# Optimization experiments

Measured on AMD Instinct MI355X. Metric: run time of the kernel, lower is better.

Reference implementation:

```python
import jax, jax.numpy as jnp
import numpy as np
from jax import lax

D_MODEL = 128

def _pad_same(x, kh, kw):
    ph, pw = kh - 1, kw - 1
    return jnp.pad(x, ((0, 0), (0, 0), (ph // 2, ph - ph // 2), (pw // 2, pw - pw // 2)))

def _conv(x, w, b):
    y = lax.conv_general_dilated(x, w, (1, 1), 'VALID', dimension_numbers=('NCHW', 'OIHW', 'NCHW'))
    return y + b[None, :, None, None]

def _group_norm(x, g, b, groups, eps=1e-5):
    N, C, H, W = x.shape
    xr = x.reshape(N, groups, -1)
    m = xr.mean(axis=2, keepdims=True)
    v = xr.var(axis=2, keepdims=True)
    xn = ((xr - m) / jnp.sqrt(v + eps)).reshape(N, C, H, W)
    return xn * g[None, :, None, None] + b[None, :, None, None]

def _maxpool(x, kh, kw):
    return lax.reduce_window(x, -jnp.inf, lax.max, (1, 1, kh, kw), (1, 1, kh, kw), 'VALID')

def _l2norm(x, axis):
    # torch F.normalize(p=2): x / max(||x||, eps)
    return x / jnp.maximum(jnp.linalg.norm(x, axis=axis, keepdims=True), 1e-12)

def _pos_encoding(S, d):
    pos = jnp.arange(S, dtype=jnp.float32)[:, None]
    div = jnp.exp(jnp.arange(0, d, 2, dtype=jnp.float32) * (-float(np.log(10000.0)) / d))
    pe = jnp.zeros((S, d), dtype=jnp.float32)
    pe = pe.at[:, 0::2].set(jnp.sin(pos * div)).at[:, 1::2].set(jnp.cos(pos * div))
    return pe

def setup_inputs() -> dict:
    key = jax.random.key(0)
    ks = jax.random.split(key, 16)
    def w(k, shape, fan_in):
        return jax.random.normal(k, shape, dtype=jnp.float32) * (1.0 / np.sqrt(fan_in))
    return {
        'x': jax.random.normal(ks[0], (1, 1024, 72, 64), dtype=jnp.float32),
        'conv1_w': w(ks[1], (32, 1, 6, 4), 1 * 6 * 4),
        'conv1_b': jnp.zeros((32,), jnp.float32),
        'gn1_g': jnp.ones((32,), jnp.float32), 'gn1_b': jnp.zeros((32,), jnp.float32),
        'conv2_w': w(ks[2], (64, 32, 6, 4), 32 * 6 * 4),
        'conv2_b': jnp.zeros((64,), jnp.float32),
        'gn2_g': jnp.ones((64,), jnp.float32), 'gn2_b': jnp.zeros((64,), jnp.float32),
        'conv3_w': w(ks[3], (128, 64, 6, 4), 64 * 6 * 4),
        'conv3_b': jnp.zeros((128,), jnp.float32),
        'gn3_g': jnp.ones((128,), jnp.float32), 'gn3_b': jnp.zeros((128,), jnp.float32),
        'fc1_w': w(ks[4], (128, 1024), 1024),
        'fc1_b': jnp.zeros((128,), jnp.float32),
        'wq': w(ks[5], (128, 128), 128), 'bq': jnp.zeros((128,), jnp.float32),
        'wk': w(ks[6], (128, 128), 128), 'bk': jnp.zeros((128,), jnp.float32),
        'wv': w(ks[7], (128, 128), 128), 'bv': jnp.zeros((128,), jnp.float32),
    }

def reference(x, conv1_w, conv1_b, gn1_g, gn1_b, conv2_w, conv2_b, gn2_g, gn2_b,
              conv3_w, conv3_b, gn3_g, gn3_b, fc1_w, fc1_b, wq, bq, wk, bk, wv, bv):
    selu = jax.nn.selu
    # x: [1, S, 72, 64] -> transpose(0,1): [S, 1, 72, 64] (S frames, 1 channel)
    h = jnp.transpose(x, (1, 0, 2, 3))
    h = _maxpool(_group_norm(selu(_conv(_pad_same(h, 6, 4), conv1_w, conv1_b)), gn1_g, gn1_b, 32), 2, 4)
    h = _maxpool(_group_norm(selu(_conv(_pad_same(h, 6, 4), conv2_w, conv2_b)), gn2_g, gn2_b, 32), 3, 4)
    h = _maxpool(_group_norm(selu(_conv(_pad_same(h, 6, 4), conv3_w, conv3_b)), gn3_g, gn3_b, 32), 3, 2)
    e = h.reshape(h.shape[0], -1)                       # [S, 1024]
    e = _l2norm(selu(e @ fc1_w.T + fc1_b), axis=1)      # [S, 128]
    S = e.shape[0]
    q = selu(e @ wq.T + bq)
    k = selu(e @ wk.T + bk)
    v = selu(e @ wv.T + bv)
    k_pos = k + _pos_encoding(S, D_MODEL)               # PE added to K only
    attn = jax.nn.softmax((q @ k_pos.T) / jnp.sqrt(jnp.float32(D_MODEL)), axis=-1)  # [S, S]
    # torch F.normalize default dim=1 on [1,S,D] -> normalize over the sequence axis
    out = _l2norm(attn @ v, axis=0) + e
    ea = _l2norm(out, axis=0)                           # [S, 128]
    # pairwise L2 distances (self-similarity matrix), then 1 - d/max(d)
    sq = jnp.sum(ea * ea, axis=1)
    d2 = jnp.maximum(sq[:, None] + sq[None, :] - 2.0 * (ea @ ea.T), 0.0)
    d = jnp.sqrt(d2 + 1e-12)
    return 1.0 - d / jnp.max(d)
```

## Files before the change

kernel.cpp:

```cpp
#include <hip/hip_runtime.h>
#include <hip/hip_bf16.h>
#include <math.h>

#define SELU_SCALE 1.0507009873554805f
#define SELU_SA    1.7580993408473766f

typedef __attribute__((ext_vector_type(8))) short short8;
typedef __attribute__((ext_vector_type(4))) short short4v;
typedef __attribute__((ext_vector_type(4))) float f32x4;

__device__ __forceinline__ float selu_f(float x){
    return x > 0.f ? SELU_SCALE * x : fmaf(SELU_SA, __expf(x), -SELU_SA);
}

__device__ __forceinline__ unsigned short bfc(float v){
    __hip_bfloat16 h = __float2bfloat16(v);
    return __builtin_bit_cast(unsigned short, h);
}
__device__ __forceinline__ float f_bf(unsigned short u){
    unsigned int x = ((unsigned int)u) << 16;
    return __builtin_bit_cast(float, x);
}

__device__ __forceinline__ float warp_sum(float v){
    #pragma unroll
    for(int o=32;o>0;o>>=1) v += __shfl_down(v,o,64);
    return v;
}
__device__ __forceinline__ float warp_max(float v){
    #pragma unroll
    for(int o=32;o>0;o>>=1) v = fmaxf(v,__shfl_down(v,o,64));
    return v;
}

__device__ __forceinline__ void block_sum2(float &a, float &b, float* sred, int nw){
    int lane = threadIdx.x & 63, w = threadIdx.x >> 6;
    a = warp_sum(a); b = warp_sum(b);
    __syncthreads();
    if(lane==0){ sred[w]=a; sred[16+w]=b; }
    __syncthreads();
    if(w==0){
        float x = (lane<nw)? sred[lane] : 0.f;
        float y = (lane<nw)? sred[16+lane] : 0.f;
        x = warp_sum(x); y = warp_sum(y);
        if(lane==0){ sred[0]=x; sred[16]=y; }
    }
    __syncthreads();
    a = sred[0]; b = sred[16];
}

__device__ __forceinline__ float block_max_f(float v, float* sred, int nw){
    int lane = threadIdx.x & 63, w = threadIdx.x >> 6;
    v = warp_max(v);
    __syncthreads();
    if(lane==0) sred[w]=v;
    __syncthreads();
    if(w==0){
        float x = (lane<nw)? sred[lane] : -INFINITY;
        x = warp_max(x);
        if(lane==0) sred[0]=x;
    }
    __syncthreads();
    return sred[0];
}

__global__ void k_prep(const float* __restrict__ f1w, const float* __restrict__ wq,
                       const float* __restrict__ wk, const float* __restrict__ wv,
                       const float* __restrict__ w1, const float* __restrict__ w2,
                       const float* __restrict__ w3,
                       float* __restrict__ wt, float* __restrict__ wqt,
                       float* __restrict__ wkt, float* __restrict__ wvt,
                       short* __restrict__ w1bf, short* __restrict__ w2bf,
                       short* __restrict__ w3bf){
    int idx = blockIdx.x*256 + threadIdx.x;
    if(idx < 131072){ int r = idx >> 10, cc = idx & 1023; wt[cc*128 + r] = f1w[idx]; return; }
    idx -= 131072;
    if(idx < 16384){ int r = idx >> 7, cc = idx & 127; wqt[cc*128 + r] = wq[idx]; return; }
    idx -= 16384;
    if(idx < 16384){ int r = idx >> 7, cc = idx & 127; wkt[cc*128 + r] = wk[idx]; return; }
    idx -= 16384;
    if(idx < 16384){ int r = idx >> 7, cc = idx & 127; wvt[cc*128 + r] = wv[idx]; return; }
    idx -= 16384;
    if(idx < 49152){
        int t = idx >> 11, rem = idx & 2047;
        int oc = rem >> 5, ic = rem & 31;
        w2bf[idx] = (short)bfc(w2[oc*768 + ic*24 + t]);
        return;
    }
    idx -= 49152;
    if(idx < 196608){
        int t = idx >> 13, rem = idx & 8191;
        int oc = rem >> 6, ic = rem & 63;
        w3bf[idx] = (short)bfc(w3[oc*1536 + ic*24 + t]);
        return;
    }
    idx -= 196608;
    if(idx < 1024){
        int oc = idx >> 5, k = idx & 31;
        w1bf[idx] = (k < 24) ? (short)bfc(w1[oc*24 + k]) : (short)0;
    }
}

__global__ __launch_bounds__(768,1) void k_conv1m(
    const float* __restrict__ x, const short* __restrict__ w1bf,
    const float* __restrict__ bias, const float* __restrict__ g,
    const float* __restrict__ be, float* __restrict__ out)
{
    int s = blockIdx.x, tid = threadIdx.x;
    int l = tid & 63, wv = tid >> 6;
    int c = l & 15, qr = l >> 4;
    __shared__ char smem[127728];
    short* sdup = (short*)smem;
    char* pmaxb = smem + 41712;
    char* pminb = smem + 83184;
    float* sredf = (float*)(smem + 124656);
    __shared__ float scsh[64];

    const float* xs = x + (size_t)s*4608;
    for(int i = tid; i < 5056; i += 768){
        int yp = i >> 6, xx = i & 63;
        unsigned long long pk = 0ull;
        if(yp >= 2 && yp < 74){
            const float* row = xs + (yp-2)*64;
            #pragma unroll
            for(int t=0;t<4;t++){
                int cp = xx + t;
                float f = (cp>=1 && cp<65) ? row[cp-1] : 0.f;
                pk |= (unsigned long long)bfc(f) << (16*t);
            }
        }
        *(unsigned long long*)((char*)sdup + yp*528 + (xx&3)*128 + (xx>>2)*8) = pk;
    }
    short8 a0 = *(const short8*)(w1bf + c*32 + qr*8);
    short8 a1 = *(const short8*)(w1bf + (16+c)*32 + qr*8);
    float bias8[8];
    #pragma unroll
    for(int t=0;t<2;t++)
        #pragma unroll
        for(int r=0;r<4;r++) bias8[t*4+r] = bias[t*16 + qr*4 + r];
    float ssum8[8], ssq8[8];
    #pragma unroll
    for(int i=0;i<8;i++){ ssum8[i]=0.f; ssq8[i]=0.f; }
    __syncthreads();

    #pragma unroll 1
    for(int u=0; u<3; u++){
        int py = wv*3 + u;
        float pmx[8], pmn[8];
        #pragma unroll
        for(int i=0;i<8;i++){ pmx[i]=-INFINITY; pmn[i]=INFINITY; }
        #pragma unroll
        for(int off=0; off<4; off++){
            const char* bb = (const char*)sdup + off*128 + c*8;
            #pragma unroll
            for(int rr=0; rr<2; rr++){
                int y = py*2 + rr;
                short4v lo = *(const short4v*)(bb + (y+2*qr)*528);
                short4v hi = *(const short4v*)(bb + (y+2*qr+1)*528);
                short8 bfrag = __builtin_shufflevector(lo, hi, 0,1,2,3,4,5,6,7);
                f32x4 d0 = __builtin_amdgcn_mfma_f32_16x16x32_bf16(a0, bfrag, (f32x4){0.f,0.f,0.f,0.f}, 0,0,0);
                f32x4 d1 = __builtin_amdgcn_mfma_f32_16x16x32_bf16(a1, bfrag, (f32x4){0.f,0.f,0.f,0.f}, 0,0,0);
                #pragma unroll
                for(int r=0;r<4;r++){
                    float v0 = selu_f(d0[r] + bias8[r]);
                    float v1 = selu_f(d1[r] + bias8[4+r]);
                    ssum8[r]   += v0; ssq8[r]   = fmaf(v0,v0,ssq8[r]);
                    ssum8[4+r] += v1; ssq8[4+r] = fmaf(v1,v1,ssq8[4+r]);
                    pmx[r]   = fmaxf(pmx[r],   v0); pmn[r]   = fminf(pmn[r],   v0);
                    pmx[4+r] = fmaxf(pmx[4+r], v1); pmn[4+r] = fminf(pmn[4+r], v1);
                }
            }
        }
        int base = (py*16 + c)*72;
        #pragma unroll
        for(int t=0;t<2;t++){
            unsigned long long mpk=0ull, npk=0ull;
            #pragma unroll
            for(int r=0;r<4;r++){
                mpk |= (unsigned long long)bfc(pmx[t*4+r]) << (16*r);
                npk |= (unsigned long long)bfc(pmn[t*4+r]) << (16*r);
            }
            *(unsigned long long*)(pmaxb + base + t*32 + qr*8) = mpk;
            *(unsigned long long*)(pminb + base + t*32 + qr*8) = npk;
        }
    }
    #pragma unroll
    for(int off=1; off<16; off<<=1){
        #pragma unroll
        for(int i=0;i<8;i++){
            ssum8[i] += __shfl_xor(ssum8[i], off);
            ssq8[i]  += __shfl_xor(ssq8[i],  off);
        }
    }
    if(c == 0){
        #pragma unroll
        for(int i=0;i<8;i++){
            sredf[((wv*4 + qr)*8 + i)*2]     = ssum8[i];
            sredf[((wv*4 + qr)*8 + i)*2 + 1] = ssq8[i];
        }
    }
    __syncthreads();
    if(tid < 32){
        int oc = tid;
        int t = oc >> 4, rem = oc & 15, q = rem >> 2, r = rem & 3;
        int i = t*4 + r;
        float sum=0.f, sq=0.f;
        for(int w=0; w<12; w++){
            sum += sredf[((w*4+q)*8+i)*2];
            sq  += sredf[((w*4+q)*8+i)*2+1];
        }
        float mean = sum*(1.f/4608.f);
        float var  = sq*(1.f/4608.f) - mean*mean;
        float inv  = rsqrtf(var + 1e-5f);
        float sc = g[oc]*inv;
        scsh[oc*2]   = sc;
        scsh[oc*2+1] = be[oc] - mean*sc;
    }
    __syncthreads();
    float* ob = out + (size_t)s*18432;
    for(int i = tid; i < 18432; i += 768){
        int oc = i / 576, wpx = i - oc*576;
        float sc = scsh[oc*2], sh = scsh[oc*2+1];
        int boff = wpx*72 + oc*2;
        float vm = f_bf(*(unsigned short*)(pmaxb + boff));
        float vn = f_bf(*(unsigned short*)(pminb + boff));
        ob[i] = fmaf(sc, (sc >= 0.f) ? vm : vn, sh);
    }
}

__global__ __launch_bounds__(512,2) void k_conv2m(
    const float* __restrict__ in, const short* __restrict__ w2bf,
    const float* __restrict__ bias, const float* __restrict__ g,
    const float* __restrict__ be, float* __restrict__ out)
{
    int s = blockIdx.x, tid = threadIdx.x;
    int l = tid & 63, wv = tid >> 6;
    int ocp = wv >> 2, yq = wv & 3;
    int xc = l & 15, qr = l >> 4;
    __shared__ short sinb[26240];
    __shared__ float sred[2][4][2][4][2][2];
    int* zp = (int*)sinb;
    for(int i=tid;i<13120;i+=512) zp[i]=0;
    __syncthreads();
    const float* ibase = in + (size_t)s*18432;
    #pragma unroll
    for(int h=0;h<2;h++){
        int ic = (wv*2+h)*2;
        #pragma unroll
        for(int k=0;k<9;k++){
            int px = l + 64*k;
            float v0 = ibase[ic*576 + px];
            float v1 = ibase[(ic+1)*576 + px];
            int R = (px>>4)+2, C = (px&15)+1;
            int key = (C>>1)&3;
            int q0 = ic>>3;
            int byteoff = (R*20+C)*64 + (((q0^key)&3)<<4) + (ic&7)*2;
            *(unsigned int*)((char*)sinb + byteoff) =
                (unsigned int)bfc(v0) | ((unsigned int)bfc(v1)<<16);
        }
    }
    __syncthreads();
    f32x4 acc[2][9];
    #pragma unroll
    for(int o=0;o<2;o++)
        #pragma unroll
        for(int yt=0;yt<9;yt++) acc[o][yt] = (f32x4){0.f,0.f,0.f,0.f};
    const short8* wb = (const short8*)w2bf;
    int arow = ocp*32 + xc;
    short8 a0 = wb[arow*4 + qr];
    short8 a1 = wb[(arow+16)*4 + qr];
    char* sb = (char*)sinb;
    for(int tap=0; tap<24; tap++){
        short8 na0, na1;
        if(tap<23){
            na0 = wb[((tap+1)*64 + arow)*4 + qr];
            na1 = wb[((tap+1)*64 + arow + 16)*4 + qr];
        }
        int kh = tap>>2, kw = tap&3;
        int C = xc + kw;
        int cb = C*64 + (((qr ^ ((C>>1)&3))&3)<<4);
        int rb = (yq*9 + kh)*1280;
        #pragma unroll
        for(int yt=0;yt<9;yt++){
            short8 bf_ = *(const short8*)(sb + rb + yt*1280 + cb);
            acc[0][yt] = __builtin_amdgcn_mfma_f32_16x16x32_bf16(a0, bf_, acc[0][yt], 0,0,0);
            acc[1][yt] = __builtin_amdgcn_mfma_f32_16x16x32_bf16(a1, bf_, acc[1][yt], 0,0,0);
        }
        a0 = na0; a1 = na1;
    }
    #pragma unroll
    for(int o=0;o<2;o++){
        int ocb = (ocp*2+o)*16 + qr*4;
        float b0 = bias[ocb], b1 = bias[ocb+1], b2 = bias[ocb+2], b3 = bias[ocb+3];
        float s0=0,q0=0,s1=0,q1=0;
        #pragma unroll
        for(int yt=0;yt<9;yt++){
            float v0=selu_f(acc[o][yt][0]+b0), v1=selu_f(acc[o][yt][1]+b1);
            float v2=selu_f(acc[o][yt][2]+b2), v3=selu_f(acc[o][yt][3]+b3);
            acc[o][yt][0]=v0; acc[o][yt][1]=v1; acc[o][yt][2]=v2; acc[o][yt][3]=v3;
            s0+=v0+v1; q0+=v0*v0+v1*v1; s1+=v2+v3; q1+=v2*v2+v3*v3;
        }
        #pragma unroll
        for(int off=1;off<16;off<<=1){
            s0+=__shfl_xor(s0,off); q0+=__shfl_xor(q0,off);
            s1+=__shfl_xor(s1,off); q1+=__shfl_xor(q1,off);
        }
        if(xc==0){
            sred[ocp][yq][o][qr][0][0]=s0; sred[ocp][yq][o][qr][0][1]=q0;
            sred[ocp][yq][o][qr][1][0]=s1; sred[ocp][yq][o][qr][1][1]=q1;
        }
    }
    __syncthreads();
    float* ob = out + (size_t)s*64*48;
    #pragma unroll
    for(int o=0;o<2;o++){
        #pragma unroll
        for(int grp=0;grp<2;grp++){
            float ts=0, tq=0;
            #pragma unroll
            for(int y2=0;y2<4;y2++){ ts += sred[ocp][y2][o][qr][grp][0]; tq += sred[ocp][y2][o][qr][grp][1]; }
            float mean = ts*(1.f/1152.f);
            float var  = tq*(1.f/1152.f) - mean*mean;
            float inv  = rsqrtf(var + 1e-5f);
            int oc0 = (ocp*2+o)*16 + qr*4 + grp*2;
            float sc0 = g[oc0]*inv,   sh0 = be[oc0]   - mean*sc0;
            float sc1 = g[oc0+1]*inv, sh1 = be[oc0+1] - mean*sc1;
            #pragma unroll
            for(int yt=0;yt<9;yt++){
                acc[o][yt][grp*2]   = acc[o][yt][grp*2]*sc0 + sh0;
                acc[o][yt][grp*2+1] = acc[o][yt][grp*2+1]*sc1 + sh1;
            }
        }
        #pragma unroll
        for(int r=0;r<4;r++){
            #pragma unroll
            for(int py=0;py<3;py++){
                float m = fmaxf(fmaxf(acc[o][3*py][r],acc[o][3*py+1][r]),acc[o][3*py+2][r]);
                m = fmaxf(m, __shfl_xor(m,1));
                m = fmaxf(m, __shfl_xor(m,2));
                if((xc&3)==0){
                    int oc = (ocp*2+o)*16 + qr*4 + r;
                    ob[(size_t)oc*48 + (yq*3+py)*4 + (xc>>2)] = m;
                }
            }
        }
    }
}

__global__ __launch_bounds__(512,2) void k_conv3m(
    const float* __restrict__ in, const short* __restrict__ w3bf,
    const float* __restrict__ bias, const float* __restrict__ g,
    const float* __restrict__ be, float* __restrict__ e0)
{
    int sq = blockIdx.x, tid = threadIdx.x;
    int l = tid & 63, wv = tid >> 6;
    int ocp = wv >> 1, sL = wv & 1;
    int c = l & 15, qr = l >> 4;
    int yl = c >> 2, xl = c & 3;
    __shared__ char smem[49152];
    short* sinb = (short*)smem;
    int* zp = (int*)smem;
    for(int i=tid;i<8704;i+=512) zp[i]=0;
    __syncthreads();
    const float* ibase = in + (size_t)sq*6144;
    for(int j=0;j<6;j++){
        int idx = tid + 512*j;
        int px = idx % 48;
        int rest = idx / 48;
        int icp = rest & 31, ss = rest >> 5;
        int ic = icp*2;
        float v0 = ibase[ss*3072 + ic*48 + px];
        float v1 = ibase[ss*3072 + (ic+1)*48 + px];
        int R = (px>>2)+2, C = (px&3)+1;
        int pos = ss*136 + R*8 + C;
        int key = ((R&1)<<2) | (C&3);
        int q0 = ic>>3;
        int byteoff = pos*128 + (((q0^key)&7)<<4) + (ic&7)*2;
        *(unsigned int*)(smem + byteoff) = (unsigned int)bfc(v0) | ((unsigned int)bfc(v1)<<16);
    }
    __syncthreads();
    f32x4 acc[2][3];
    #pragma unroll
    for(int o=0;o<2;o++)
        #pragma unroll
        for(int yt=0;yt<3;yt++) acc[o][yt] = (f32x4){0.f,0.f,0.f,0.f};
    const short8* wb = (const short8*)w3bf;
    int arow = ocp*32 + c;
    char* sb = smem + sL*17408;
    short8 a0 = wb[arow*8 + qr];
    short8 a1 = wb[(arow+16)*8 + qr];
    for(int t2=0; t2<48; t2++){
        short8 na0, na1;
        if(t2<47){
            int nt = t2+1;
            na0 = wb[((nt>>1)*128 + arow)*8 + (nt&1)*4 + qr];
            na1 = wb[((nt>>1)*128 + arow + 16)*8 + (nt&1)*4 + qr];
        }
        int tap = t2>>1, ks = t2&1;
        int kh = tap>>2, kw = tap&3;
        int C = xl + kw;
        int q0 = ks*4 + qr;
        #pragma unroll
        for(int yt=0;yt<3;yt++){
            int R = yt*4 + yl + kh;
            int key = ((R&1)<<2) | (C&3);
            short8 bf_ = *(const short8*)(sb + (R*8+C)*128 + (((q0^key)&7)<<4));
            acc[0][yt] = __builtin_amdgcn_mfma_f32_16x16x32_bf16(a0, bf_, acc[0][yt], 0,0,0);
            acc[1][yt] = __builtin_amdgcn_mfma_f32_16x16x32_bf16(a1, bf_, acc[1][yt], 0,0,0);
        }
        a0 = na0; a1 = na1;
    }
    #pragma unroll
    for(int o=0;o<2;o++){
        int ocb = (ocp*2+o)*16 + qr*4;
        float b0 = bias[ocb], b1 = bias[ocb+1], b2 = bias[ocb+2], b3 = bias[ocb+3];
        float ssum=0.f, ssq=0.f;
        #pragma unroll
        for(int yt=0;yt<3;yt++){
            float v0=selu_f(acc[o][yt][0]+b0), v1=selu_f(acc[o][yt][1]+b1);
            float v2=selu_f(acc[o][yt][2]+b2), v3=selu_f(acc[o][yt][3]+b3);
            acc[o][yt][0]=v0; acc[o][yt][1]=v1; acc[o][yt][2]=v2; acc[o][yt][3]=v3;
            ssum += v0+v1+v2+v3; ssq += v0*v0+v1*v1+v2*v2+v3*v3;
        }
        #pragma unroll
        for(int off=1;off<16;off<<=1){ ssum+=__shfl_xor(ssum,off); ssq+=__shfl_xor(ssq,off); }
        float mean = ssum*(1.f/192.f);
        float var  = ssq*(1.f/192.f) - mean*mean;
        float inv  = rsqrtf(var + 1e-5f);
        #pragma unroll
        for(int r=0;r<4;r++){
            int oc = ocb + r;
            float sc = g[oc]*inv, sh = be[oc] - mean*sc;
            #pragma unroll
            for(int yt=0;yt<3;yt++) acc[o][yt][r] = acc[o][yt][r]*sc + sh;
        }
    }
    __syncthreads();
    float* scr = (float*)smem + wv*1536;
    #pragma unroll
    for(int o=0;o<2;o++)
        #pragma unroll
        for(int yt=0;yt<3;yt++)
            #pragma unroll
            for(int r=0;r<4;r++){
                int px = (yt*4+yl)*4 + xl;
                scr[o*768 + (qr*4+r)*48 + px] = acc[o][yt][r];
            }
    __syncthreads();
    float* sr = (float*)smem + wv*1536 + (l>>5)*768 + ((l>>1)&15)*48;
    int x2 = l&1;
    float* eo = e0 + (size_t)(sq*2+sL)*1024 + ((size_t)(ocp*2 + (l>>5))*16 + ((l>>1)&15))*8;
    #pragma unroll
    for(int py=0;py<4;py++){
        float m = sr[(py*3)*4 + x2*2];
        m = fmaxf(m, sr[(py*3)*4 + x2*2+1]);
        m = fmaxf(m, sr[(py*3+1)*4 + x2*2]);
        m = fmaxf(m, sr[(py*3+1)*4 + x2*2+1]);
        m = fmaxf(m, sr[(py*3+2)*4 + x2*2]);
        m = fmaxf(m, sr[(py*3+2)*4 + x2*2+1]);
        eo[py*2 + x2] = m;
    }
}

__global__ __launch_bounds__(256) void k_fcqkv(
    const float* __restrict__ e0, const float* __restrict__ wt,
    const float* __restrict__ bias, float* __restrict__ e,
    const float* __restrict__ wqt, const float* __restrict__ bq,
    const float* __restrict__ wkt, const float* __restrict__ bk,
    const float* __restrict__ wvt, const float* __restrict__ bv,
    float* __restrict__ q, float* __restrict__ kp, float* __restrict__ v)
{
    int s = blockIdx.x, tid = threadIdx.x;
    int j = tid & 127, half = tid >> 7;
    __shared__ float se[1024];
    __shared__ float sp[2][128];
    __shared__ float sred[2];
    __shared__ float se2[128];
    __shared__ float sp3[3][2][128];
    for(int i=tid;i<1024;i+=256) se[i] = e0[(size_t)s*1024+i];
    __syncthreads();
    float acc = half ? 0.f : bias[j];
    const float* wp = wt + (size_t)half*512*128 + j;
    const float* sep = se + half*512;
    #pragma unroll 8
    for(int i=0;i<512;i++) acc += sep[i]*wp[(size_t)i*128];
    sp[half][j] = acc;
    __syncthreads();
    if(half==0){
        float vv = selu_f(sp[0][j]+sp[1][j]);
        float a = vv*vv;
        #pragma unroll
        for(int o=1;o<64;o<<=1) a += __shfl_xor(a,o);
        if((j&63)==0) sred[j>>6]=a;
    }
    __syncthreads();
    if(half==0){
        float den = fmaxf(sqrtf(sred[0]+sred[1]), 1e-12f);
        float vv = selu_f(sp[0][j]+sp[1][j]);
        float ev = vv/den;
        se2[j] = ev;
        e[(size_t)s*128+j] = ev;
    }
    __syncthreads();
    float aq = half?0.f:bq[j], ak = half?0.f:bk[j], av = half?0.f:bv[j];
    int i0 = half*64;
    #pragma unroll 8
    for(int i=i0;i<i0+64;i++){
        float f = se2[i];
        aq += f*wqt[i*128+j];
        ak += f*wkt[i*128+j];
        av += f*wvt[i*128+j];
    }
    sp3[0][half][j]=aq; sp3[1][half][j]=ak; sp3[2][half][j]=av;
    __syncthreads();
    if(half==0){
        float vq = selu_f(sp3[0][0][j]+sp3[0][1][j]);
        float vk = selu_f(sp3[1][0][j]+sp3[1][1][j]);
        float vv = selu_f(sp3[2][0][j]+sp3[2][1][j]);
        int i2 = j & ~1;
        float div = __expf(-(float)i2 * 0.07195578412155481f);
        float ang = (float)s * div;
        float pe = (j & 1) ? cosf(ang) : sinf(ang);
        q[(size_t)s*128+j]  = vq;
        kp[(size_t)s*128+j] = vk + pe;
        v[(size_t)s*128+j]  = vv;
    }
}

__global__ __launch_bounds__(256) void k_attnav(
    const float* __restrict__ q, const float* __restrict__ kp,
    const float* __restrict__ v, float* __restrict__ av)
{
    int s = blockIdx.x, tid = threadIdx.x;
    __shared__ float sq_[128];
    __shared__ float sredm[32];
    __shared__ float spb[1024];
    __shared__ float spart[2][128];
    if(tid < 128) sq_[tid] = q[(size_t)s*128+tid];
    __syncthreads();
    float val[4];
    const float4* qr = (const float4*)sq_;
    #pragma unroll
    for(int k2=0;k2<4;k2++){
        int t = tid + k2*256;
        const float4* kr = (const float4*)(kp + (size_t)t*128);
        float acc=0.f;
        #pragma unroll 8
        for(int i=0;i<32;i++){
            float4 a=qr[i], b=kr[i];
            acc += a.x*b.x + a.y*b.y + a.z*b.z + a.w*b.w;
        }
        val[k2] = acc * 0.08838834764831845f;
    }
    float m = fmaxf(fmaxf(val[0],val[1]), fmaxf(val[2],val[3]));
    m = block_max_f(m,sredm,4);
    float lsum=0.f, dummy=0.f;
    #pragma unroll
    for(int k2=0;k2<4;k2++){ val[k2]=__expf(val[k2]-m); lsum+=val[k2]; }
    block_sum2(lsum,dummy,sredm,4);
    float invs = 1.f/lsum;
    #pragma unroll
    for(int k2=0;k2<4;k2++) spb[tid + k2*256] = val[k2]*invs;
    __syncthreads();
    int j = tid & 127, half = tid >> 7;
    float acc=0.f;
    int t0 = half*512;
    for(int t=t0;t<t0+512;t++) acc += spb[t]*v[(size_t)t*128+j];
    spart[half][j] = acc;
    __syncthreads();
    if(half==0) av[(size_t)s*128+j] = spart[0][j] + spart[1][j];
}

__global__ __launch_bounds__(256) void k_colpipe(
    const float* __restrict__ av, const float* __restrict__ e, float* __restrict__ ea)
{
    int j = blockIdx.x, t = threadIdx.x;
    __shared__ float sred[4];
    float v[4];
    float ss = 0.f;
    #pragma unroll
    for(int k=0;k<4;k++){
        v[k] = av[(size_t)(t + 256*k)*128 + j];
        ss += v[k]*v[k];
    }
    #pragma unroll
    for(int off=1;off<64;off<<=1) ss += __shfl_xor(ss,off);
    int lane = t & 63, w = t >> 6;
    if(lane==0) sred[w]=ss;
    __syncthreads();
    float n1 = fmaxf(sqrtf(sred[0]+sred[1]+sred[2]+sred[3]), 1e-12f);
    __syncthreads();
    float ss2 = 0.f;
    #pragma unroll
    for(int k=0;k<4;k++){
        float o = v[k]/n1 + e[(size_t)(t + 256*k)*128 + j];
        v[k] = o;
        ss2 += o*o;
    }
    #pragma unroll
    for(int off=1;off<64;off<<=1) ss2 += __shfl_xor(ss2,off);
    if(lane==0) sred[w]=ss2;
    __syncthreads();
    float n2 = fmaxf(sqrtf(sred[0]+sred[1]+sred[2]+sred[3]), 1e-12f);
    #pragma unroll
    for(int k=0;k<4;k++) ea[(size_t)(t + 256*k)*128 + j] = v[k]/n2;
}

__global__ __launch_bounds__(128) void k_sq(const float* __restrict__ ea, float* __restrict__ sq){
    int s = blockIdx.x, j = threadIdx.x;
    __shared__ float sred[32];
    float v = ea[(size_t)s*128+j];
    float a=v*v, b=0.f;
    block_sum2(a,b,sred,2);
    if(j==0) sq[s]=a;
}

__global__ __launch_bounds__(256) void k_gram(
    const float* __restrict__ ea, const float* __restrict__ sq,
    float* __restrict__ d2, unsigned int* __restrict__ maxbits)
{
    int j0 = blockIdx.x*32, i0 = blockIdx.y*32, tid = threadIdx.x;
    __shared__ float sa[32*128];
    __shared__ float sb[32*128];
    __shared__ float sred[32];
    for(int idx=tid;idx<4096;idx+=256){
        sa[idx] = ea[(size_t)i0*128 + idx];
        sb[idx] = ea[(size_t)j0*128 + idx];
    }
    __syncthreads();
    float lm = 0.f;
    #pragma unroll
    for(int k2=0;k2<4;k2++){
        int p = tid + k2*256;
        int li = p>>5, lj = p&31;
        const float4* A = (const float4*)(sa + li*128);
        const float4* B = (const float4*)(sb + lj*128);
        float acc=0.f;
        #pragma unroll 8
        for(int i=0;i<32;i++){
            float4 a=A[i], b=B[i];
            acc += a.x*b.x + a.y*b.y + a.z*b.z + a.w*b.w;
        }
        float dd = fmaxf(sq[i0+li] + sq[j0+lj] - 2.f*acc, 0.f);
        d2[(size_t)(i0+li)*1024 + j0+lj] = dd;
        lm = fmaxf(lm, dd);
    }
    lm = block_max_f(lm,sred,4);
    if(tid==0) atomicMax(maxbits, __float_as_uint(lm));
}

__global__ __launch_bounds__(256) void k_final(
    const float* __restrict__ d2, const unsigned int* __restrict__ maxbits, float* __restrict__ out)
{
    int idx = blockIdx.x*256 + threadIdx.x;
    float md = sqrtf(__uint_as_float(*maxbits) + 1e-12f);
    out[idx] = 1.f - sqrtf(d2[idx] + 1e-12f)/md;
}

extern "C" void kernel_launch(void* const* d_in, const int* in_sizes, int n_in,
                              void* d_out, int out_size, void* d_ws, size_t ws_size,
                              hipStream_t stream)
{
    const float* x   = (const float*)d_in[0];
    const float* c1w = (const float*)d_in[1];  const float* c1b = (const float*)d_in[2];
    const float* g1g = (const float*)d_in[3];  const float* g1b = (const float*)d_in[4];
    const float* c2w = (const float*)d_in[5];  const float* c2b = (const float*)d_in[6];
    const float* g2g = (const float*)d_in[7];  const float* g2b = (const float*)d_in[8];
    const float* c3w = (const float*)d_in[9];  const float* c3b = (const float*)d_in[10];
    const float* g3g = (const float*)d_in[11]; const float* g3b = (const float*)d_in[12];
    const float* f1w = (const float*)d_in[13]; const float* f1b = (const float*)d_in[14];
    const float* wq  = (const float*)d_in[15]; const float* bq  = (const float*)d_in[16];
    const float* wk  = (const float*)d_in[17]; const float* bk  = (const float*)d_in[18];
    const float* wv  = (const float*)d_in[19]; const float* bv  = (const float*)d_in[20];

    float* W = (float*)d_ws;
    float* e0   = W;
    float* avb  = W + 2097152;
    float* eab  = W + 2228224;
    float* d2b  = W + 2359296;
    float* buf1 = W;
    float* buf2 = W + 18874368;
    float* wt   = W + 22020096;
    float* wqt  = W + 22151168;
    float* wkt  = W + 22167552;
    float* wvt  = W + 22183936;
    float* eb   = W + 22200320;
    float* qb   = W + 22331392;
    float* kpb  = W + 22462464;
    float* vb   = W + 22593536;
    float* sqb  = W + 22724608;
    unsigned int* maxb = (unsigned int*)(W + 22725632);
    short* w2bf = (short*)(W + 22725648);
    short* w3bf = (short*)(W + 22750224);
    short* w1bf = (short*)(W + 22848528);

    k_prep<<<1670,256,0,stream>>>(f1w, wq, wk, wv, c1w, c2w, c3w,
                                  wt, wqt, wkt, wvt, w1bf, w2bf, w3bf);

    k_conv1m<<<1024,768,0,stream>>>(x, w1bf, c1b, g1g, g1b, buf1);
    k_conv2m<<<1024,512,0,stream>>>(buf1, w2bf, c2b, g2g, g2b, buf2);
    k_conv3m<<<512,512,0,stream>>>(buf2, w3bf, c3b, g3g, g3b, e0);

    k_fcqkv<<<1024,256,0,stream>>>(e0, wt, f1b, eb, wqt,bq, wkt,bk, wvt,bv, qb,kpb,vb);
    k_attnav<<<1024,256,0,stream>>>(qb, kpb, vb, avb);

    hipMemsetAsync(maxb, 0, 4, stream);
    k_colpipe<<<128,256,0,stream>>>(avb, eb, eab);
    k_sq<<<1024,128,0,stream>>>(eab, sqb);
    k_gram<<<dim3(32,32),256,0,stream>>>(eab, sqb, d2b, maxb);
    k_final<<<4096,256,0,stream>>>(d2b, maxb, (float*)d_out);
}
```

Before: 387.9 us.

## Batch four sequence rows per block in FC/QKV and attention, fold row norms into gram

The fc1/QKV and attention kernels now handle four sequence positions per 512-thread block, so each weight, key and value load is reused across four rows instead of one. The column-normalisation kernel uses 1024 threads with one element each. The separate squared-norm kernel is removed and its sums are computed inside the gram tile kernel from shared memory. The aim is less redundant global traffic on weights and K/V plus one fewer launch, at the cost of fewer blocks (256) in the middle stages and some repeated norm work across gram tiles.

```diff
diff --git a/kernel.cpp b/kernel.cpp
--- a/kernel.cpp
+++ b/kernel.cpp
@@ -22,46 +22,10 @@
     return __builtin_bit_cast(float, x);
 }
 
-__device__ __forceinline__ float warp_sum(float v){
-    #pragma unroll
-    for(int o=32;o>0;o>>=1) v += __shfl_down(v,o,64);
-    return v;
-}
 __device__ __forceinline__ float warp_max(float v){
     #pragma unroll
     for(int o=32;o>0;o>>=1) v = fmaxf(v,__shfl_down(v,o,64));
     return v;
-}
-
-__device__ __forceinline__ void block_sum2(float &a, float &b, float* sred, int nw){
-    int lane = threadIdx.x & 63, w = threadIdx.x >> 6;
-    a = warp_sum(a); b = warp_sum(b);
-    __syncthreads();
-    if(lane==0){ sred[w]=a; sred[16+w]=b; }
-    __syncthreads();
-    if(w==0){
-        float x = (lane<nw)? sred[lane] : 0.f;
-        float y = (lane<nw)? sred[16+lane] : 0.f;
-        x = warp_sum(x); y = warp_sum(y);
-        if(lane==0){ sred[0]=x; sred[16]=y; }
-    }
-    __syncthreads();
-    a = sred[0]; b = sred[16];
-}
-
-__device__ __forceinline__ float block_max_f(float v, float* sred, int nw){
-    int lane = threadIdx.x & 63, w = threadIdx.x >> 6;
-    v = warp_max(v);
-    __syncthreads();
-    if(lane==0) sred[w]=v;
-    __syncthreads();
-    if(w==0){
-        float x = (lane<nw)? sred[lane] : -INFINITY;
-        x = warp_max(x);
-        if(lane==0) sred[0]=x;
-    }
-    __syncthreads();
-    return sred[0];
 }
 
 __global__ void k_prep(const float* __restrict__ f1w, const float* __restrict__ wq,
@@ -462,7 +426,7 @@
     }
 }
 
-__global__ __launch_bounds__(256) void k_fcqkv(
+__global__ __launch_bounds__(512) void k_fcqkv(
     const float* __restrict__ e0, const float* __restrict__ wt,
     const float* __restrict__ bias, float* __restrict__ e,
     const float* __restrict__ wqt, const float* __restrict__ bq,
@@ -470,169 +434,202 @@
     const float* __restrict__ wvt, const float* __restrict__ bv,
     float* __restrict__ q, float* __restrict__ kp, float* __restrict__ v)
 {
-    int s = blockIdx.x, tid = threadIdx.x;
-    int j = tid & 127, half = tid >> 7;
-    __shared__ float se[1024];
-    __shared__ float sp[2][128];
-    __shared__ float sred[2];
-    __shared__ float se2[128];
-    __shared__ float sp3[3][2][128];
-    for(int i=tid;i<1024;i+=256) se[i] = e0[(size_t)s*1024+i];
-    __syncthreads();
-    float acc = half ? 0.f : bias[j];
-    const float* wp = wt + (size_t)half*512*128 + j;
-    const float* sep = se + half*512;
-    #pragma unroll 8
-    for(int i=0;i<512;i++) acc += sep[i]*wp[(size_t)i*128];
-    sp[half][j] = acc;
-    __syncthreads();
-    if(half==0){
-        float vv = selu_f(sp[0][j]+sp[1][j]);
-        float a = vv*vv;
-        #pragma unroll
-        for(int o=1;o<64;o<<=1) a += __shfl_xor(a,o);
-        if((j&63)==0) sred[j>>6]=a;
-    }
-    __syncthreads();
-    if(half==0){
-        float den = fmaxf(sqrtf(sred[0]+sred[1]), 1e-12f);
-        float vv = selu_f(sp[0][j]+sp[1][j]);
-        float ev = vv/den;
-        se2[j] = ev;
-        e[(size_t)s*128+j] = ev;
-    }
-    __syncthreads();
-    float aq = half?0.f:bq[j], ak = half?0.f:bk[j], av = half?0.f:bv[j];
-    int i0 = half*64;
-    #pragma unroll 8
-    for(int i=i0;i<i0+64;i++){
-        float f = se2[i];
-        aq += f*wqt[i*128+j];
-        ak += f*wkt[i*128+j];
-        av += f*wvt[i*128+j];
-    }
-    sp3[0][half][j]=aq; sp3[1][half][j]=ak; sp3[2][half][j]=av;
-    __syncthreads();
-    if(half==0){
-        float vq = selu_f(sp3[0][0][j]+sp3[0][1][j]);
-        float vk = selu_f(sp3[1][0][j]+sp3[1][1][j]);
-        float vv = selu_f(sp3[2][0][j]+sp3[2][1][j]);
-        int i2 = j & ~1;
-        float div = __expf(-(float)i2 * 0.07195578412155481f);
-        float ang = (float)s * div;
-        float pe = (j & 1) ? cosf(ang) : sinf(ang);
-        q[(size_t)s*128+j]  = vq;
-        kp[(size_t)s*128+j] = vk + pe;
-        v[(size_t)s*128+j]  = vv;
-    }
-}
-
-__global__ __launch_bounds__(256) void k_attnav(
+    int s0 = blockIdx.x*4, tid = threadIdx.x;
+    int j = tid & 127, q4 = tid >> 7;
+    __shared__ float se[4][1024];
+    __shared__ float sp[4][4][128];
+    __shared__ float sredn[4][2];
+    __shared__ float se2[4][128];
+    __shared__ float sp3[3][4][4][128];
+    for(int i=tid;i<4096;i+=512){
+        int sl = i >> 10, ii = i & 1023;
+        se[sl][ii] = e0[(size_t)(s0+sl)*1024 + ii];
+    }
+    __syncthreads();
+    float acc[4] = {0.f,0.f,0.f,0.f};
+    const float* wp = wt + (size_t)q4*256*128 + j;
+    const int ibase = q4*256;
+    #pragma unroll 4
+    for(int i=0;i<256;i++){
+        float w = wp[(size_t)i*128];
+        #pragma unroll
+        for(int sl=0;sl<4;sl++) acc[sl] = fmaf(se[sl][ibase+i], w, acc[sl]);
+    }
+    #pragma unroll
+    for(int sl=0;sl<4;sl++) sp[sl][q4][j] = acc[sl];
+    __syncthreads();
+    int sl2 = q4, lane = tid & 63, wv_ = tid >> 6;
+    float vfc = selu_f(bias[j] + sp[sl2][0][j] + sp[sl2][1][j] + sp[sl2][2][j] + sp[sl2][3][j]);
+    float a = vfc*vfc;
+    #pragma unroll
+    for(int o=1;o<64;o<<=1) a += __shfl_xor(a, o);
+    if(lane==0) sredn[sl2][wv_&1] = a;
+    __syncthreads();
+    float den = fmaxf(sqrtf(sredn[sl2][0]+sredn[sl2][1]), 1e-12f);
+    float ev = vfc/den;
+    se2[sl2][j] = ev;
+    e[(size_t)(s0+sl2)*128 + j] = ev;
+    __syncthreads();
+    float aq[4]={0,0,0,0}, ak[4]={0,0,0,0}, av[4]={0,0,0,0};
+    int i0b = q4*32;
+    #pragma unroll 4
+    for(int i=0;i<32;i++){
+        float wqv = wqt[(i0b+i)*128 + j];
+        float wkv = wkt[(i0b+i)*128 + j];
+        float wvv = wvt[(i0b+i)*128 + j];
+        #pragma unroll
+        for(int sl=0;sl<4;sl++){
+            float f = se2[sl][i0b+i];
+            aq[sl] = fmaf(f, wqv, aq[sl]);
+            ak[sl] = fmaf(f, wkv, ak[sl]);
+            av[sl] = fmaf(f, wvv, av[sl]);
+        }
+    }
+    #pragma unroll
+    for(int sl=0;sl<4;sl++){
+        sp3[0][sl][q4][j] = aq[sl];
+        sp3[1][sl][q4][j] = ak[sl];
+        sp3[2][sl][q4][j] = av[sl];
+    }
+    __syncthreads();
+    float vq = selu_f(bq[j] + sp3[0][sl2][0][j]+sp3[0][sl2][1][j]+sp3[0][sl2][2][j]+sp3[0][sl2][3][j]);
+    float vk = selu_f(bk[j] + sp3[1][sl2][0][j]+sp3[1][sl2][1][j]+sp3[1][sl2][2][j]+sp3[1][sl2][3][j]);
+    float vv = selu_f(bv[j] + sp3[2][sl2][0][j]+sp3[2][sl2][1][j]+sp3[2][sl2][2][j]+sp3[2][sl2][3][j]);
+    int i2 = j & ~1;
+    float dv = __expf(-(float)i2 * 0.07195578412155481f);
+    float ang = (float)(s0+sl2) * dv;
+    float pe = (j & 1) ? cosf(ang) : sinf(ang);
+    q[(size_t)(s0+sl2)*128+j]  = vq;
+    kp[(size_t)(s0+sl2)*128+j] = vk + pe;
+    v[(size_t)(s0+sl2)*128+j]  = vv;
+}
+
+__global__ __launch_bounds__(512) void k_attnav(
     const float* __restrict__ q, const float* __restrict__ kp,
     const float* __restrict__ v, float* __restrict__ av)
 {
-    int s = blockIdx.x, tid = threadIdx.x;
-    __shared__ float sq_[128];
-    __shared__ float sredm[32];
-    __shared__ float spb[1024];
-    __shared__ float spart[2][128];
-    if(tid < 128) sq_[tid] = q[(size_t)s*128+tid];
-    __syncthreads();
-    float val[4];
-    const float4* qr = (const float4*)sq_;
-    #pragma unroll
-    for(int k2=0;k2<4;k2++){
-        int t = tid + k2*256;
+    int s0 = blockIdx.x*4, tid = threadIdx.x;
+    __shared__ float4 sq4[4][32];
+    __shared__ float p[4][1024];
+    __shared__ float spart[4][4][128];
+    __shared__ float smx[4][2], ssm[4][2];
+    ((float*)sq4)[tid] = q[(size_t)s0*128 + tid];
+    __syncthreads();
+    #pragma unroll
+    for(int h=0;h<2;h++){
+        int t = tid + h*512;
         const float4* kr = (const float4*)(kp + (size_t)t*128);
-        float acc=0.f;
-        #pragma unroll 8
+        float d[4] = {0.f,0.f,0.f,0.f};
+        #pragma unroll 4
         for(int i=0;i<32;i++){
-            float4 a=qr[i], b=kr[i];
-            acc += a.x*b.x + a.y*b.y + a.z*b.z + a.w*b.w;
-        }
-        val[k2] = acc * 0.08838834764831845f;
-    }
-    float m = fmaxf(fmaxf(val[0],val[1]), fmaxf(val[2],val[3]));
-    m = block_max_f(m,sredm,4);
-    float lsum=0.f, dummy=0.f;
-    #pragma unroll
-    for(int k2=0;k2<4;k2++){ val[k2]=__expf(val[k2]-m); lsum+=val[k2]; }
-    block_sum2(lsum,dummy,sredm,4);
-    float invs = 1.f/lsum;
-    #pragma unroll
-    for(int k2=0;k2<4;k2++) spb[tid + k2*256] = val[k2]*invs;
-    __syncthreads();
-    int j = tid & 127, half = tid >> 7;
-    float acc=0.f;
-    int t0 = half*512;
-    for(int t=t0;t<t0+512;t++) acc += spb[t]*v[(size_t)t*128+j];
-    spart[half][j] = acc;
-    __syncthreads();
-    if(half==0) av[(size_t)s*128+j] = spart[0][j] + spart[1][j];
-}
-
-__global__ __launch_bounds__(256) void k_colpipe(
+            float4 kv = kr[i];
+            #pragma unroll
+            for(int sl=0;sl<4;sl++){
+                float4 qv = sq4[sl][i];
+                d[sl] += kv.x*qv.x + kv.y*qv.y + kv.z*qv.z + kv.w*qv.w;
+            }
+        }
+        #pragma unroll
+        for(int sl=0;sl<4;sl++) p[sl][t] = d[sl]*0.08838834764831845f;
+    }
+    __syncthreads();
+    int sl2 = tid>>7, t2 = tid&127, lane = tid&63, wv_ = tid>>6;
+    float vals[8];
+    float m = -INFINITY;
+    #pragma unroll
+    for(int k=0;k<8;k++){ vals[k] = p[sl2][t2 + k*128]; m = fmaxf(m, vals[k]); }
+    #pragma unroll
+    for(int o=1;o<64;o<<=1) m = fmaxf(m, __shfl_xor(m,o));
+    if(lane==0) smx[sl2][wv_&1] = m;
+    __syncthreads();
+    m = fmaxf(smx[sl2][0], smx[sl2][1]);
+    float lsum = 0.f;
+    #pragma unroll
+    for(int k=0;k<8;k++){ vals[k] = __expf(vals[k]-m); lsum += vals[k]; }
+    #pragma unroll
+    for(int o=1;o<64;o<<=1) lsum += __shfl_xor(lsum,o);
+    if(lane==0) ssm[sl2][wv_&1] = lsum;
+    __syncthreads();
+    float invs = 1.f/(ssm[sl2][0]+ssm[sl2][1]);
+    #pragma unroll
+    for(int k=0;k<8;k++) p[sl2][t2+k*128] = vals[k]*invs;
+    __syncthreads();
+    int j = tid & 127, q4 = tid >> 7;
+    float acc[4] = {0,0,0,0};
+    int t0 = q4*256;
+    #pragma unroll 2
+    for(int t=t0;t<t0+256;t++){
+        float vv = v[(size_t)t*128 + j];
+        #pragma unroll
+        for(int sl=0;sl<4;sl++) acc[sl] = fmaf(p[sl][t], vv, acc[sl]);
+    }
+    #pragma unroll
+    for(int sl=0;sl<4;sl++) spart[sl][q4][j] = acc[sl];
+    __syncthreads();
+    av[(size_t)(s0+sl2)*128 + j] = spart[sl2][0][j]+spart[sl2][1][j]+spart[sl2][2][j]+spart[sl2][3][j];
+}
+
+__global__ __launch_bounds__(1024) void k_colpipe(
     const float* __restrict__ av, const float* __restrict__ e, float* __restrict__ ea)
 {
     int j = blockIdx.x, t = threadIdx.x;
-    __shared__ float sred[4];
-    float v[4];
-    float ss = 0.f;
-    #pragma unroll
-    for(int k=0;k<4;k++){
-        v[k] = av[(size_t)(t + 256*k)*128 + j];
-        ss += v[k]*v[k];
-    }
+    __shared__ float sred[16];
+    int lane = t & 63, w = t >> 6;
+    float vv = av[(size_t)t*128 + j];
+    float ss = vv*vv;
     #pragma unroll
     for(int off=1;off<64;off<<=1) ss += __shfl_xor(ss,off);
-    int lane = t & 63, w = t >> 6;
     if(lane==0) sred[w]=ss;
     __syncthreads();
-    float n1 = fmaxf(sqrtf(sred[0]+sred[1]+sred[2]+sred[3]), 1e-12f);
-    __syncthreads();
-    float ss2 = 0.f;
-    #pragma unroll
-    for(int k=0;k<4;k++){
-        float o = v[k]/n1 + e[(size_t)(t + 256*k)*128 + j];
-        v[k] = o;
-        ss2 += o*o;
-    }
+    float tot = 0.f;
+    #pragma unroll
+    for(int i=0;i<16;i++) tot += sred[i];
+    float n1 = fmaxf(sqrtf(tot), 1e-12f);
+    __syncthreads();
+    float o = vv/n1 + e[(size_t)t*128 + j];
+    float ss2 = o*o;
     #pragma unroll
     for(int off=1;off<64;off<<=1) ss2 += __shfl_xor(ss2,off);
     if(lane==0) sred[w]=ss2;
     __syncthreads();
-    float n2 = fmaxf(sqrtf(sred[0]+sred[1]+sred[2]+sred[3]), 1e-12f);
-    #pragma unroll
-    for(int k=0;k<4;k++) ea[(size_t)(t + 256*k)*128 + j] = v[k]/n2;
-}
-
-__global__ __launch_bounds__(128) void k_sq(const float* __restrict__ ea, float* __restrict__ sq){
-    int s = blockIdx.x, j = threadIdx.x;
-    __shared__ float sred[32];
-    float v = ea[(size_t)s*128+j];
-    float a=v*v, b=0.f;
-    block_sum2(a,b,sred,2);
-    if(j==0) sq[s]=a;
+    float tot2 = 0.f;
+    #pragma unroll
+    for(int i=0;i<16;i++) tot2 += sred[i];
+    float n2 = fmaxf(sqrtf(tot2), 1e-12f);
+    ea[(size_t)t*128 + j] = o/n2;
 }
 
 __global__ __launch_bounds__(256) void k_gram(
-    const float* __restrict__ ea, const float* __restrict__ sq,
+    const float* __restrict__ ea,
     float* __restrict__ d2, unsigned int* __restrict__ maxbits)
 {
     int j0 = blockIdx.x*32, i0 = blockIdx.y*32, tid = threadIdx.x;
     __shared__ float sa[32*128];
     __shared__ float sb[32*128];
-    __shared__ float sred[32];
+    __shared__ float sredm[32];
+    __shared__ float sqa[32], sqb[32];
     for(int idx=tid;idx<4096;idx+=256){
         sa[idx] = ea[(size_t)i0*128 + idx];
         sb[idx] = ea[(size_t)j0*128 + idx];
     }
     __syncthreads();
+    {
+        int r = tid>>3, seg = tid&7;
+        const float* A = sa + r*128 + seg*16;
+        const float* B = sb + r*128 + seg*16;
+        float pa=0.f, pb=0.f;
+        #pragma unroll
+        for(int i=0;i<16;i++){ pa = fmaf(A[i],A[i],pa); pb = fmaf(B[i],B[i],pb); }
+        #pragma unroll
+        for(int o=1;o<8;o<<=1){ pa += __shfl_xor(pa,o); pb += __shfl_xor(pb,o); }
+        if(seg==0){ sqa[r]=pa; sqb[r]=pb; }
+    }
+    __syncthreads();
     float lm = 0.f;
     #pragma unroll
     for(int k2=0;k2<4;k2++){
-        int p = tid + k2*256;
-        int li = p>>5, lj = p&31;
+        int pp = tid + k2*256;
+        int li = pp>>5, lj = pp&31;
         const float4* A = (const float4*)(sa + li*128);
         const float4* B = (const float4*)(sb + lj*128);
         float acc=0.f;
@@ -641,12 +638,18 @@
             float4 a=A[i], b=B[i];
             acc += a.x*b.x + a.y*b.y + a.z*b.z + a.w*b.w;
         }
-        float dd = fmaxf(sq[i0+li] + sq[j0+lj] - 2.f*acc, 0.f);
+        float dd = fmaxf(sqa[li] + sqb[lj] - 2.f*acc, 0.f);
         d2[(size_t)(i0+li)*1024 + j0+lj] = dd;
         lm = fmaxf(lm, dd);
     }
-    lm = block_max_f(lm,sred,4);
-    if(tid==0) atomicMax(maxbits, __float_as_uint(lm));
+    lm = warp_max(lm);
+    __syncthreads();
+    if((tid&63)==0) sredm[tid>>6]=lm;
+    __syncthreads();
+    if(tid==0){
+        float mm = fmaxf(fmaxf(sredm[0],sredm[1]),fmaxf(sredm[2],sredm[3]));
+        atomicMax(maxbits, __float_as_uint(mm));
+    }
 }
 
 __global__ __launch_bounds__(256) void k_final(
@@ -688,7 +691,6 @@
     float* qb   = W + 22331392;
     float* kpb  = W + 22462464;
     float* vb   = W + 22593536;
-    float* sqb  = W + 22724608;
     unsigned int* maxb = (unsigned int*)(W + 22725632);
     short* w2bf = (short*)(W + 22725648);
     short* w3bf = (short*)(W + 22750224);
@@ -701,12 +703,11 @@
     k_conv2m<<<1024,512,0,stream>>>(buf1, w2bf, c2b, g2g, g2b, buf2);
     k_conv3m<<<512,512,0,stream>>>(buf2, w3bf, c3b, g3g, g3b, e0);
 
-    k_fcqkv<<<1024,256,0,stream>>>(e0, wt, f1b, eb, wqt,bq, wkt,bk, wvt,bv, qb,kpb,vb);
-    k_attnav<<<1024,256,0,stream>>>(qb, kpb, vb, avb);
+    k_fcqkv<<<256,512,0,stream>>>(e0, wt, f1b, eb, wqt,bq, wkt,bk, wvt,bv, qb,kpb,vb);
+    k_attnav<<<256,512,0,stream>>>(qb, kpb, vb, avb);
 
     hipMemsetAsync(maxb, 0, 4, stream);
-    k_colpipe<<<128,256,0,stream>>>(avb, eb, eab);
-    k_sq<<<1024,128,0,stream>>>(eab, sqb);
-    k_gram<<<dim3(32,32),256,0,stream>>>(eab, sqb, d2b, maxb);
+    k_colpipe<<<128,1024,0,stream>>>(avb, eb, eab);
+    k_gram<<<dim3(32,32),256,0,stream>>>(eab, d2b, maxb);
     k_final<<<4096,256,0,stream>>>(d2b, maxb, (float*)d_out);
 }
```

After: 367.9 us. -5.2%, faster.
